# Kernel tuning notes

Measured on AMD Instinct MI355X. Metric: run time of the kernel, lower is better.

The kernel has to match this reference:

```python
import jax, jax.numpy as jnp
import numpy as np

DK = 64
DROPOUT_P = 0.1


def setup_inputs() -> dict:
    key = jax.random.key(0)
    kq, kk, kv, km = jax.random.split(key, 4)
    B, S, D = 16, 2048, 64
    q = jax.random.normal(kq, (B, S, D), dtype=jnp.float32)
    k = jax.random.normal(kk, (B, S, D), dtype=jnp.float32)
    v = jax.random.normal(kv, (B, S, D), dtype=jnp.float32)
    attn_mask = jax.random.randint(km, (S, S), 0, 2, dtype=jnp.int32)
    return {"q": q, "k": k, "v": v, "attn_mask": attn_mask}


def reference(q, k, v, attn_mask):
    # q = q / sqrt(dk)
    qs = q * (1.0 / np.sqrt(DK)).astype(np.float32)
    # dots: [B, S_q, S_k]
    dots = jnp.einsum("bqd,bkd->bqk", qs, k)
    # mask: 0 -> -inf, 1 -> 0 (additive)
    add_mask = jnp.where(attn_mask == 0, -jnp.inf, 0.0).astype(dots.dtype)
    dots = dots + add_mask  # broadcast [S,S] over batch
    attn = jax.nn.softmax(dots, axis=-1)
    # inverted dropout, train mode, fixed key for determinism
    keep = jax.random.bernoulli(jax.random.key(42), 1.0 - DROPOUT_P, attn.shape)
    attn = jnp.where(keep, attn * (1.0 / (1.0 - DROPOUT_P)), 0.0)
    out = jnp.einsum("bqk,bkd->bqd", attn, v)
    return out
```

## Files before the change

kernel.cpp:

```cpp
#include <hip/hip_runtime.h>

#define BATCH 16
#define SEQ   2048
#define DIM   64
#define TQ    64
#define TK    64
#define NTHREADS 256
#define NROWS    (BATCH * SEQ)
#define OUTELEMS (NROWS * DIM)

typedef short bf16x8 __attribute__((ext_vector_type(8)));
typedef float f32x4 __attribute__((ext_vector_type(4)));

__device__ __forceinline__ int ldsoff(int row) {
  return row * 72 + 16 * (row >> 2);
}
#define LDS_SZ (64 * 72 + 16 * 16)

__device__ __forceinline__ unsigned tf_bits(unsigned f) {
  unsigned x0 = 0u;
  unsigned x1 = f;
  const unsigned ks1 = 42u;
  const unsigned ks2 = 0x1BD11BDAu ^ 42u;
  x1 += ks1;
#define TF_R(r) { x0 += x1; x1 = __builtin_amdgcn_alignbit(x1, x1, 32u - (r)); x1 ^= x0; }
  TF_R(13) TF_R(15) TF_R(26) TF_R(6)
  x0 += ks1; x1 += ks2 + 1u;
  TF_R(17) TF_R(29) TF_R(16) TF_R(24)
  x0 += ks2; x1 += 2u;
  TF_R(13) TF_R(15) TF_R(26) TF_R(6)
  x1 += ks1 + 3u;
  TF_R(17) TF_R(29) TF_R(16) TF_R(24)
  x0 += ks1; x1 += ks2 + 4u;
  TF_R(13) TF_R(15) TF_R(26) TF_R(6)
  x0 += ks2; x1 += 5u;
#undef TF_R
  return x0 ^ x1;
}
#define KEEP_THRESH 0xE6666600u

__device__ __forceinline__ unsigned pack_bf16x2(float lo, float hi) {
  const unsigned l = (__float_as_uint(lo) + 0x8000u) >> 16;
  const unsigned h = (__float_as_uint(hi) + 0x8000u) & 0xFFFF0000u;
  return h | l;
}

#define WS_L0 0
#define WS_L1 32768
#define WS_O1 65536
#define WS_NEED ((size_t)(WS_O1 + OUTELEMS) * 4)

template <int SPLIT>
__global__ __launch_bounds__(NTHREADS, 4)
void attn_fwd(const float* __restrict__ q, const float* __restrict__ k,
              const float* __restrict__ v, const int* __restrict__ mask,
              float* __restrict__ out, float* __restrict__ ws) {
  __shared__ unsigned short KP[LDS_SZ];
  __shared__ unsigned short VT[LDS_SZ];

  const int t    = threadIdx.x;
  const int w    = t >> 6;
  const int lane = t & 63;
  const int tx   = lane & 15;
  const int quad = lane >> 4;

  int bid = blockIdx.x;
  const int half = SPLIT ? (bid >> 9) : 0;
  bid &= 511;
  const int bb = bid >> 5;
  const int q0 = (bid & 31) * TQ;
  const int qw = q0 + 16 * w;
  const int kt0 = SPLIT ? half * (SEQ / TK / 2) : 0;
  const int ktN = SPLIT ? (SEQ / TK / 2) : (SEQ / TK);

  const float qscale = 0.125f * 1.44269504088896340736f;

  bf16x8 aq[2];
  {
    const float* qr = q + ((size_t)bb * SEQ + qw + tx) * DIM + quad * 8;
#pragma unroll
    for (int ks = 0; ks < 2; ++ks) {
      const float4 f0 = *(const float4*)(qr + ks * 32);
      const float4 f1 = *(const float4*)(qr + ks * 32 + 4);
      union { unsigned u[4]; bf16x8 v; } a;
      a.u[0] = pack_bf16x2(f0.x * qscale, f0.y * qscale);
      a.u[1] = pack_bf16x2(f0.z * qscale, f0.w * qscale);
      a.u[2] = pack_bf16x2(f1.x * qscale, f1.y * qscale);
      a.u[3] = pack_bf16x2(f1.z * qscale, f1.w * qscale);
      aq[ks] = a.v;
    }
  }

  float lrun[4] = {0.f, 0.f, 0.f, 0.f};
  f32x4 oacc[4];
#pragma unroll
  for (int nt = 0; nt < 4; ++nt) oacc[nt] = (f32x4){0.f, 0.f, 0.f, 0.f};

  const int srow0 = t >> 4;
  const int sdd   = (t & 15) * 4;
  const float* kb = k + (size_t)bb * SEQ * DIM;
  const float* vb = v + (size_t)bb * SEQ * DIM;

  float4 kreg[4], vreg[4];
  {
    const size_t off0 = (size_t)kt0 * TK * DIM;
#pragma unroll
    for (int p = 0; p < 4; ++p) {
      const size_t ro = off0 + (size_t)(p * 16 + srow0) * DIM + sdd;
      kreg[p] = *(const float4*)(kb + ro);
      vreg[p] = *(const float4*)(vb + ro);
    }
  }

  const int* mbase = mask + (size_t)(qw + quad * 4) * SEQ + tx;
  const unsigned fbase0 = (unsigned)(bb * SEQ + qw + quad * 4) * (unsigned)SEQ + (unsigned)tx;

#pragma unroll 1
  for (int kt = kt0; kt < kt0 + ktN; ++kt) {
    const int k0 = kt * TK;

    __syncthreads();

#pragma unroll
    for (int p = 0; p < 4; ++p) {
      const int rr = p * 16 + srow0;
      uint2 kk;
      kk.x = pack_bf16x2(kreg[p].x, kreg[p].y);
      kk.y = pack_bf16x2(kreg[p].z, kreg[p].w);
      *(uint2*)&KP[ldsoff(rr) + sdd] = kk;
    }
    {
      const float* vp = (const float*)vreg;
#pragma unroll
      for (int c = 0; c < 4; ++c) {
        uint2 tv;
        tv.x = pack_bf16x2(vp[0 * 4 + c], vp[1 * 4 + c]);
        tv.y = pack_bf16x2(vp[2 * 4 + c], vp[3 * 4 + c]);
        *(uint2*)&VT[ldsoff(sdd + c) + 4 * srow0] = tv;
      }
    }
    __syncthreads();

    if (kt + 1 < kt0 + ktN) {
      const size_t off = (size_t)(k0 + TK) * DIM;
#pragma unroll
      for (int p = 0; p < 4; ++p) {
        const size_t ro = off + (size_t)(p * 16 + srow0) * DIM + sdd;
        kreg[p] = *(const float4*)(kb + ro);
        vreg[p] = *(const float4*)(vb + ro);
      }
    }

    int mv[4][4];
    const int* mp0 = mbase + k0;
#pragma unroll
    for (int reg = 0; reg < 4; ++reg)
#pragma unroll
      for (int nt = 0; nt < 4; ++nt)
        mv[nt][reg] = mp0[(size_t)reg * SEQ + nt * 16];

    f32x4 qk[4];
#pragma unroll
    for (int nt = 0; nt < 4; ++nt) {
      f32x4 c = (f32x4){0.f, 0.f, 0.f, 0.f};
#pragma unroll
      for (int ks = 0; ks < 2; ++ks) {
        const bf16x8 b = *(const bf16x8*)&KP[ldsoff(nt * 16 + tx) + ks * 32 + quad * 8];
        c = __builtin_amdgcn_mfma_f32_16x16x32_bf16(aq[ks], b, c, 0, 0, 0);
      }
      qk[nt] = c;
    }

    __syncthreads();

    const unsigned fb = fbase0 + (unsigned)k0;
#pragma unroll
    for (int reg = 0; reg < 4; ++reg) {
      float pd[4];
      float ls = 0.0f;
#pragma unroll
      for (int nt = 0; nt < 4; ++nt) {
        const float s = mv[nt][reg] ? qk[nt][reg] : -1e30f;
        const float e = __builtin_amdgcn_exp2f(s);
        ls += e;
        const unsigned bits = tf_bits(fb + (unsigned)(reg * SEQ + nt * 16));
        pd[nt] = (bits < KEEP_THRESH) ? e : 0.0f;
      }
      lrun[reg] += ls;
      uint2 pw;
      pw.x = pack_bf16x2(pd[0], pd[1]);
      pw.y = pack_bf16x2(pd[2], pd[3]);
      *(uint2*)&KP[ldsoff(16 * w + quad * 4 + reg) + 4 * tx] = pw;
    }

#pragma unroll
    for (int ks = 0; ks < 2; ++ks) {
      const bf16x8 ap = *(const bf16x8*)&KP[ldsoff(16 * w + tx) + ks * 32 + quad * 8];
#pragma unroll
      for (int nt = 0; nt < 4; ++nt) {
        const bf16x8 bv = *(const bf16x8*)&VT[ldsoff(nt * 16 + tx) + ks * 32 + quad * 8];
        oacc[nt] = __builtin_amdgcn_mfma_f32_16x16x32_bf16(ap, bv, oacc[nt], 0, 0, 0);
      }
    }
  }

  float lred[4];
#pragma unroll
  for (int reg = 0; reg < 4; ++reg) {
    float ls = lrun[reg];
    ls += __shfl_xor(ls, 1);
    ls += __shfl_xor(ls, 2);
    ls += __shfl_xor(ls, 4);
    ls += __shfl_xor(ls, 8);
    lred[reg] = ls;
  }
  if (SPLIT) {
    float* optr = half ? (ws + WS_O1) : out;
    float* lptr = ws + (half ? WS_L1 : WS_L0);
    if (tx == 0) {
#pragma unroll
      for (int reg = 0; reg < 4; ++reg)
        lptr[bb * SEQ + qw + quad * 4 + reg] = lred[reg];
    }
    float* ob = optr + ((size_t)bb * SEQ + qw) * DIM;
#pragma unroll
    for (int nt = 0; nt < 4; ++nt)
#pragma unroll
      for (int reg = 0; reg < 4; ++reg)
        ob[(size_t)(quad * 4 + reg) * DIM + nt * 16 + tx] = oacc[nt][reg];
  } else {
    float* ob = out + ((size_t)bb * SEQ + qw) * DIM;
#pragma unroll
    for (int nt = 0; nt < 4; ++nt)
#pragma unroll
      for (int reg = 0; reg < 4; ++reg)
        ob[(size_t)(quad * 4 + reg) * DIM + nt * 16 + tx] =
            oacc[nt][reg] * ((1.0f / 0.9f) / lred[reg]);
  }
}

__global__ __launch_bounds__(NTHREADS)
void combine(float* __restrict__ out, const float* __restrict__ ws) {
  const int gid = blockIdx.x * NTHREADS + threadIdx.x;
  const int row = gid >> 6;
  const float den = 0.9f * (ws[WS_L0 + row] + ws[WS_L1 + row]);
  out[gid] = (out[gid] + ws[WS_O1 + gid]) / den;
}

extern "C" void kernel_launch(void* const* d_in, const int* in_sizes, int n_in,
                              void* d_out, int out_size, void* d_ws, size_t ws_size,
                              hipStream_t stream) {
  const float* q = (const float*)d_in[0];
  const float* k = (const float*)d_in[1];
  const float* v = (const float*)d_in[2];
  const int* mask = (const int*)d_in[3];
  float* out = (float*)d_out;
  float* ws = (float*)d_ws;
  if (ws_size >= WS_NEED) {
    hipLaunchKernelGGL(attn_fwd<1>, dim3(1024), dim3(NTHREADS), 0, stream,
                       q, k, v, mask, out, ws);
    hipLaunchKernelGGL(combine, dim3(OUTELEMS / NTHREADS), dim3(NTHREADS), 0, stream,
                       out, ws);
  } else {
    hipLaunchKernelGGL(attn_fwd<0>, dim3(512), dim3(NTHREADS), 0, stream,
                       q, k, v, mask, out, ws);
  }
}
```

Before: 242.5 us.

## Pre-pack K/V into bf16 MFMA fragment layout and drop LDS staging

Adds a `convert_kv` pre-pass that converts K and V to bf16, laid out in the exact per-lane MFMA fragment order, in workspace. The attention kernel now loads those fragments straight from global memory into registers. This removes the per-tile LDS staging of K/V and most `__syncthreads` calls; only a small, wave-local P buffer stays in LDS. Key columns are permuted so each thread reads its mask values as one contiguous int4, and the dropout counter indices are remapped to match. The two split halves now merge through atomicAdd into a zeroed output and a row-sum buffer, at the cost of two memsets, an extra pass over K/V, and atomic traffic.

```diff
diff --git a/kernel.cpp b/kernel.cpp
--- a/kernel.cpp
+++ b/kernel.cpp
@@ -3,8 +3,6 @@
 #define BATCH 16
 #define SEQ   2048
 #define DIM   64
-#define TQ    64
-#define TK    64
 #define NTHREADS 256
 #define NROWS    (BATCH * SEQ)
 #define OUTELEMS (NROWS * DIM)
@@ -45,18 +43,43 @@
   return h | l;
 }
 
-#define WS_L0 0
-#define WS_L1 32768
-#define WS_O1 65536
-#define WS_NEED ((size_t)(WS_O1 + OUTELEMS) * 4)
-
-template <int SPLIT>
+#define WS_KF 0
+#define WS_VF 1048576
+#define WS_L  2097152
+
+__global__ __launch_bounds__(NTHREADS)
+void convert_kv(const float* __restrict__ k, const float* __restrict__ v,
+                unsigned* __restrict__ ws) {
+  const unsigned gid = blockIdx.x * NTHREADS + threadIdx.x;
+  const unsigned e = gid & 262143u;
+  const int lane = e & 63;
+  const int ks = (e >> 6) & 1, nt = (e >> 7) & 3, kt = (e >> 9) & 31, b = e >> 14;
+  const int tx = lane & 15, quad = lane >> 4;
+  uint4 wout;
+  if (gid < 262144u) {
+    const float* src = k + ((size_t)b * SEQ + kt * 64 + 4 * tx + nt) * DIM
+                         + ks * 32 + quad * 8;
+    const float4 f0 = *(const float4*)src;
+    const float4 f1 = *(const float4*)(src + 4);
+    wout.x = pack_bf16x2(f0.x, f0.y); wout.y = pack_bf16x2(f0.z, f0.w);
+    wout.z = pack_bf16x2(f1.x, f1.y); wout.w = pack_bf16x2(f1.z, f1.w);
+    *(uint4*)(ws + WS_KF + (size_t)e * 4) = wout;
+  } else {
+    const float* src = v + ((size_t)b * SEQ + kt * 64 + ks * 32 + quad * 8) * DIM
+                         + nt * 16 + tx;
+    const float a0 = src[0 * DIM], a1 = src[1 * DIM], a2 = src[2 * DIM], a3 = src[3 * DIM];
+    const float a4 = src[4 * DIM], a5 = src[5 * DIM], a6 = src[6 * DIM], a7 = src[7 * DIM];
+    wout.x = pack_bf16x2(a0, a1); wout.y = pack_bf16x2(a2, a3);
+    wout.z = pack_bf16x2(a4, a5); wout.w = pack_bf16x2(a6, a7);
+    *(uint4*)(ws + WS_VF + (size_t)e * 4) = wout;
+  }
+}
+
 __global__ __launch_bounds__(NTHREADS, 4)
-void attn_fwd(const float* __restrict__ q, const float* __restrict__ k,
-              const float* __restrict__ v, const int* __restrict__ mask,
-              float* __restrict__ out, float* __restrict__ ws) {
-  __shared__ unsigned short KP[LDS_SZ];
-  __shared__ unsigned short VT[LDS_SZ];
+void attn_fwd(const float* __restrict__ q, const unsigned* __restrict__ ws,
+              const int* __restrict__ mask, float* __restrict__ out,
+              float* __restrict__ lsum) {
+  __shared__ unsigned short PS[LDS_SZ];
 
   const int t    = threadIdx.x;
   const int w    = t >> 6;
@@ -65,13 +88,12 @@
   const int quad = lane >> 4;
 
   int bid = blockIdx.x;
-  const int half = SPLIT ? (bid >> 9) : 0;
+  const int half = bid >> 9;
   bid &= 511;
   const int bb = bid >> 5;
-  const int q0 = (bid & 31) * TQ;
+  const int q0 = (bid & 31) * 64;
   const int qw = q0 + 16 * w;
-  const int kt0 = SPLIT ? half * (SEQ / TK / 2) : 0;
-  const int ktN = SPLIT ? (SEQ / TK / 2) : (SEQ / TK);
+  const int kt0 = half * 16;
 
   const float qscale = 0.125f * 1.44269504088896340736f;
 
@@ -96,111 +118,74 @@
 #pragma unroll
   for (int nt = 0; nt < 4; ++nt) oacc[nt] = (f32x4){0.f, 0.f, 0.f, 0.f};
 
-  const int srow0 = t >> 4;
-  const int sdd   = (t & 15) * 4;
-  const float* kb = k + (size_t)bb * SEQ * DIM;
-  const float* vb = v + (size_t)bb * SEQ * DIM;
-
-  float4 kreg[4], vreg[4];
-  {
-    const size_t off0 = (size_t)kt0 * TK * DIM;
-#pragma unroll
-    for (int p = 0; p < 4; ++p) {
-      const size_t ro = off0 + (size_t)(p * 16 + srow0) * DIM + sdd;
-      kreg[p] = *(const float4*)(kb + ro);
-      vreg[p] = *(const float4*)(vb + ro);
-    }
-  }
-
-  const int* mbase = mask + (size_t)(qw + quad * 4) * SEQ + tx;
-  const unsigned fbase0 = (unsigned)(bb * SEQ + qw + quad * 4) * (unsigned)SEQ + (unsigned)tx;
+  const unsigned* kfb = ws + WS_KF + (size_t)(bb * 32) * 2048 + (size_t)lane * 4;
+  const unsigned* vfb = ws + WS_VF + (size_t)(bb * 32) * 2048 + (size_t)lane * 4;
+  const int* mbase = mask + (size_t)(qw + quad * 4) * SEQ + 4 * tx;
+  const unsigned fbase0 = (unsigned)(bb * SEQ + qw + quad * 4) * (unsigned)SEQ
+                          + (unsigned)(4 * tx);
 
 #pragma unroll 1
-  for (int kt = kt0; kt < kt0 + ktN; ++kt) {
-    const int k0 = kt * TK;
-
-    __syncthreads();
-
-#pragma unroll
-    for (int p = 0; p < 4; ++p) {
-      const int rr = p * 16 + srow0;
-      uint2 kk;
-      kk.x = pack_bf16x2(kreg[p].x, kreg[p].y);
-      kk.y = pack_bf16x2(kreg[p].z, kreg[p].w);
-      *(uint2*)&KP[ldsoff(rr) + sdd] = kk;
-    }
-    {
-      const float* vp = (const float*)vreg;
-#pragma unroll
-      for (int c = 0; c < 4; ++c) {
-        uint2 tv;
-        tv.x = pack_bf16x2(vp[0 * 4 + c], vp[1 * 4 + c]);
-        tv.y = pack_bf16x2(vp[2 * 4 + c], vp[3 * 4 + c]);
-        *(uint2*)&VT[ldsoff(sdd + c) + 4 * srow0] = tv;
-      }
-    }
-    __syncthreads();
-
-    if (kt + 1 < kt0 + ktN) {
-      const size_t off = (size_t)(k0 + TK) * DIM;
-#pragma unroll
-      for (int p = 0; p < 4; ++p) {
-        const size_t ro = off + (size_t)(p * 16 + srow0) * DIM + sdd;
-        kreg[p] = *(const float4*)(kb + ro);
-        vreg[p] = *(const float4*)(vb + ro);
-      }
-    }
-
-    int mv[4][4];
-    const int* mp0 = mbase + k0;
+  for (int kt = kt0; kt < kt0 + 16; ++kt) {
+    const int k0 = kt * 64;
+
+    int4 mv[4];
 #pragma unroll
     for (int reg = 0; reg < 4; ++reg)
-#pragma unroll
-      for (int nt = 0; nt < 4; ++nt)
-        mv[nt][reg] = mp0[(size_t)reg * SEQ + nt * 16];
+      mv[reg] = *(const int4*)(mbase + (size_t)reg * SEQ + k0);
+
+    const unsigned* kfp = kfb + (size_t)kt * 2048;
+    bf16x8 kf[4][2];
+#pragma unroll
+    for (int nt = 0; nt < 4; ++nt)
+#pragma unroll
+      for (int ks = 0; ks < 2; ++ks)
+        kf[nt][ks] = *(const bf16x8*)(kfp + (nt * 2 + ks) * 256);
 
     f32x4 qk[4];
 #pragma unroll
     for (int nt = 0; nt < 4; ++nt) {
       f32x4 c = (f32x4){0.f, 0.f, 0.f, 0.f};
 #pragma unroll
-      for (int ks = 0; ks < 2; ++ks) {
-        const bf16x8 b = *(const bf16x8*)&KP[ldsoff(nt * 16 + tx) + ks * 32 + quad * 8];
-        c = __builtin_amdgcn_mfma_f32_16x16x32_bf16(aq[ks], b, c, 0, 0, 0);
-      }
+      for (int ks = 0; ks < 2; ++ks)
+        c = __builtin_amdgcn_mfma_f32_16x16x32_bf16(aq[ks], kf[nt][ks], c, 0, 0, 0);
       qk[nt] = c;
     }
 
-    __syncthreads();
+    const unsigned* vfp = vfb + (size_t)kt * 2048;
+    bf16x8 vf[4][2];
+#pragma unroll
+    for (int nt = 0; nt < 4; ++nt)
+#pragma unroll
+      for (int ks = 0; ks < 2; ++ks)
+        vf[nt][ks] = *(const bf16x8*)(vfp + (nt * 2 + ks) * 256);
 
     const unsigned fb = fbase0 + (unsigned)k0;
 #pragma unroll
     for (int reg = 0; reg < 4; ++reg) {
+      const int* mreg = (const int*)&mv[reg];
       float pd[4];
       float ls = 0.0f;
 #pragma unroll
       for (int nt = 0; nt < 4; ++nt) {
-        const float s = mv[nt][reg] ? qk[nt][reg] : -1e30f;
+        const float s = mreg[nt] ? qk[nt][reg] : -1e30f;
         const float e = __builtin_amdgcn_exp2f(s);
         ls += e;
-        const unsigned bits = tf_bits(fb + (unsigned)(reg * SEQ + nt * 16));
+        const unsigned bits = tf_bits(fb + (unsigned)(reg * SEQ) + (unsigned)nt);
         pd[nt] = (bits < KEEP_THRESH) ? e : 0.0f;
       }
       lrun[reg] += ls;
       uint2 pw;
       pw.x = pack_bf16x2(pd[0], pd[1]);
       pw.y = pack_bf16x2(pd[2], pd[3]);
-      *(uint2*)&KP[ldsoff(16 * w + quad * 4 + reg) + 4 * tx] = pw;
+      *(uint2*)&PS[ldsoff(16 * w + quad * 4 + reg) + 4 * tx] = pw;
     }
 
 #pragma unroll
     for (int ks = 0; ks < 2; ++ks) {
-      const bf16x8 ap = *(const bf16x8*)&KP[ldsoff(16 * w + tx) + ks * 32 + quad * 8];
-#pragma unroll
-      for (int nt = 0; nt < 4; ++nt) {
-        const bf16x8 bv = *(const bf16x8*)&VT[ldsoff(nt * 16 + tx) + ks * 32 + quad * 8];
-        oacc[nt] = __builtin_amdgcn_mfma_f32_16x16x32_bf16(ap, bv, oacc[nt], 0, 0, 0);
-      }
+      const bf16x8 ap = *(const bf16x8*)&PS[ldsoff(16 * w + tx) + ks * 32 + quad * 8];
+#pragma unroll
+      for (int nt = 0; nt < 4; ++nt)
+        oacc[nt] = __builtin_amdgcn_mfma_f32_16x16x32_bf16(ap, vf[nt][ks], oacc[nt], 0, 0, 0);
     }
   }
 
@@ -214,37 +199,24 @@
     ls += __shfl_xor(ls, 8);
     lred[reg] = ls;
   }
-  if (SPLIT) {
-    float* optr = half ? (ws + WS_O1) : out;
-    float* lptr = ws + (half ? WS_L1 : WS_L0);
-    if (tx == 0) {
-#pragma unroll
-      for (int reg = 0; reg < 4; ++reg)
-        lptr[bb * SEQ + qw + quad * 4 + reg] = lred[reg];
-    }
-    float* ob = optr + ((size_t)bb * SEQ + qw) * DIM;
-#pragma unroll
-    for (int nt = 0; nt < 4; ++nt)
-#pragma unroll
-      for (int reg = 0; reg < 4; ++reg)
-        ob[(size_t)(quad * 4 + reg) * DIM + nt * 16 + tx] = oacc[nt][reg];
-  } else {
-    float* ob = out + ((size_t)bb * SEQ + qw) * DIM;
-#pragma unroll
-    for (int nt = 0; nt < 4; ++nt)
-#pragma unroll
-      for (int reg = 0; reg < 4; ++reg)
-        ob[(size_t)(quad * 4 + reg) * DIM + nt * 16 + tx] =
-            oacc[nt][reg] * ((1.0f / 0.9f) / lred[reg]);
-  }
+  if (tx == 0) {
+#pragma unroll
+    for (int reg = 0; reg < 4; ++reg)
+      atomicAdd(&lsum[bb * SEQ + qw + quad * 4 + reg], lred[reg]);
+  }
+  float* ob = out + ((size_t)bb * SEQ + qw) * DIM;
+#pragma unroll
+  for (int nt = 0; nt < 4; ++nt)
+#pragma unroll
+    for (int reg = 0; reg < 4; ++reg)
+      atomicAdd(&ob[(size_t)(quad * 4 + reg) * DIM + nt * 16 + tx], oacc[nt][reg]);
 }
 
 __global__ __launch_bounds__(NTHREADS)
-void combine(float* __restrict__ out, const float* __restrict__ ws) {
+void combine(float* __restrict__ out, const float* __restrict__ lsum) {
   const int gid = blockIdx.x * NTHREADS + threadIdx.x;
   const int row = gid >> 6;
-  const float den = 0.9f * (ws[WS_L0 + row] + ws[WS_L1 + row]);
-  out[gid] = (out[gid] + ws[WS_O1 + gid]) / den;
+  out[gid] = out[gid] * (1.0f / (0.9f * lsum[row]));
 }
 
 extern "C" void kernel_launch(void* const* d_in, const int* in_sizes, int n_in,
@@ -255,14 +227,13 @@
   const float* v = (const float*)d_in[2];
   const int* mask = (const int*)d_in[3];
   float* out = (float*)d_out;
-  float* ws = (float*)d_ws;
-  if (ws_size >= WS_NEED) {
-    hipLaunchKernelGGL(attn_fwd<1>, dim3(1024), dim3(NTHREADS), 0, stream,
-                       q, k, v, mask, out, ws);
-    hipLaunchKernelGGL(combine, dim3(OUTELEMS / NTHREADS), dim3(NTHREADS), 0, stream,
-                       out, ws);
-  } else {
-    hipLaunchKernelGGL(attn_fwd<0>, dim3(512), dim3(NTHREADS), 0, stream,
-                       q, k, v, mask, out, ws);
-  }
-}
+  unsigned* ws = (unsigned*)d_ws;
+
+  hipMemsetAsync(out, 0, (size_t)out_size * 4, stream);
+  hipMemsetAsync((float*)d_ws + WS_L, 0, (size_t)NROWS * 4, stream);
+  hipLaunchKernelGGL(convert_kv, dim3(2048), dim3(NTHREADS), 0, stream, k, v, ws);
+  hipLaunchKernelGGL(attn_fwd, dim3(1024), dim3(NTHREADS), 0, stream,
+                     q, ws, mask, out, (float*)d_ws + WS_L);
+  hipLaunchKernelGGL(combine, dim3(OUTELEMS / NTHREADS), dim3(NTHREADS), 0, stream,
+                     out, (const float*)d_ws + WS_L);
+}
```

New measurement: 243.1 us. No clear change (+0.3%).
